# Optimization experiments

Measured on AMD Instinct MI355X. Metric: run time of the kernel, lower is better.

## Reference

```python
import jax, jax.numpy as jnp
import numpy as np

B, OBS, H, M, L1, T, A = 16384, 376, 512, 8, 3, 50, 17  # L1 = num_layers - 1
LOG_SQRT_2PI = 0.5 * np.log(2.0 * np.pi).astype(np.float32)


def setup_inputs() -> dict:
    key = jax.random.key(0)
    ks = jax.random.split(key, 16)
    s = lambda fan: 1.0 / np.sqrt(fan).astype(np.float32)
    return {
        "x": jax.random.normal(ks[0], (B, OBS), jnp.float32),
        "task_idx": jax.random.randint(ks[1], (B,), 0, T, jnp.int64),
        "enc_W1": jax.random.normal(ks[2], (OBS, H), jnp.float32) * s(OBS),
        "enc_b1": jnp.zeros((H,), jnp.float32),
        "enc_W2": jax.random.normal(ks[3], (H, H), jnp.float32) * s(H),
        "enc_b2": jnp.zeros((H,), jnp.float32),
        "task_emb": jax.random.normal(ks[4], (T, H), jnp.float32),
        "a_rW": jax.random.normal(ks[5], (L1, H, M * M), jnp.float32) * s(H),
        "a_rb": jnp.zeros((L1, M * M), jnp.float32),
        "c_rW": jax.random.normal(ks[6], (L1, H, M * M), jnp.float32) * s(H),
        "c_rb": jnp.zeros((L1, M * M), jnp.float32),
        "a_W": jax.random.normal(ks[7], (L1, M, H, H), jnp.float32) * s(H),
        "a_b": jnp.zeros((L1, M, H), jnp.float32),
        "a_Wf": jax.random.normal(ks[8], (M, H, A), jnp.float32) * 0.01,
        "a_bf": jnp.zeros((M, A), jnp.float32),
        "c_W": jax.random.normal(ks[9], (L1, M, H, H), jnp.float32) * s(H),
        "c_b": jnp.zeros((L1, M, H), jnp.float32),
        "c_Wf": jax.random.normal(ks[10], (M, H, 1), jnp.float32) * s(H),
        "c_bf": jnp.zeros((M, 1), jnp.float32),
        "actor_logstd": jnp.zeros((1, A), jnp.float32),
    }


def _routing(context, rW, rb):
    # context: [B,H]; rW: [L1,H,M*M] -> list of [B,M,M] softmax routing probs
    rel = jax.nn.relu(context)
    probs = []
    for l in range(L1):
        logits = (rel @ rW[l] + rb[l]).reshape(-1, M, M)
        probs.append(jax.nn.softmax(logits, axis=2))
    return probs


def _base(f_s, probs, W, b, Wf, bf):
    # f_s: [B,H]; W: [L1,M,H,H]; Wf: [M,H,out]
    g = jnp.broadcast_to(f_s[:, None, :], (f_s.shape[0], M, H))  # [B,M,H]
    for l in range(L1):
        outs = jax.nn.relu(jnp.einsum("bmh,mhk->bmk", g, W[l]) + b[l])  # [B,M,H]
        g = jnp.einsum("bij,bjh->bih", probs[l], outs)  # soft combine
    final = jnp.einsum("bmh,mhk->bmk", g, Wf) + bf  # [B,M,out]
    return final.sum(axis=1)


def reference(x, task_idx, enc_W1, enc_b1, enc_W2, enc_b2, task_emb,
              a_rW, a_rb, c_rW, c_rb, a_W, a_b, a_Wf, a_bf,
              c_W, c_b, c_Wf, c_bf, actor_logstd):
    f_s = jnp.tanh(jnp.tanh(x @ enc_W1 + enc_b1) @ enc_W2 + enc_b2)  # [B,H]
    h_z = task_emb[task_idx]  # [B,H]
    context = f_s * h_z

    value = _base(f_s, _routing(context, c_rW, c_rb), c_W, c_b, c_Wf, c_bf)  # [B,1]
    mean = _base(f_s, _routing(context, a_rW, a_rb), a_W, a_b, a_Wf, a_bf)   # [B,A]

    # deterministic action (sample=False): action = mean
    logstd = jnp.broadcast_to(actor_logstd, mean.shape)
    log_prob = (-logstd - LOG_SQRT_2PI).sum(axis=1)          # N.log_prob(mean).sum(1)
    entropy = (0.5 + LOG_SQRT_2PI + logstd).sum(axis=1)
    # concat (action, log_prob, entropy, value) -> [B, A+3]
    return jnp.concatenate([mean, log_prob[:, None], entropy[:, None], value], axis=1)
```

## Files before the change

### kernel.cpp

```cpp
#include <hip/hip_runtime.h>
#include <hip/hip_bf16.h>

typedef float f32x4 __attribute__((ext_vector_type(4)));
typedef float f32x2 __attribute__((ext_vector_type(2)));
typedef int   i32x4 __attribute__((ext_vector_type(4)));
typedef int   i32x8 __attribute__((ext_vector_type(8)));

#define LOG_SQRT_2PI 0.91893853320467274f

static constexpr int BSZ  = 16384;
static constexpr int OBSN = 376;
static constexpr int HD   = 512;
static constexpr int NACT = 17;

__device__ __forceinline__ unsigned char f2fp8(float v) {
  return (unsigned char)(__builtin_amdgcn_cvt_pk_fp8_f32(v, v, 0, false) & 0xFF);
}

__device__ __forceinline__ void gl16(const unsigned char* g, unsigned char* l) {
  __builtin_amdgcn_global_load_lds((const __attribute__((address_space(1))) void*)g,
                                   (__attribute__((address_space(3))) void*)l, 16, 0, 0);
}

__device__ __forceinline__ void xcd_map(int id, int gx, int gy, int& bx, int& by, int& bz) {
  int p = id & 7, l = id >> 3;
  bx = l % gx;
  int g = (l / gx) * 8 + p;
  by = g % gy;
  bz = g / gy;
}


__global__ void k_cvt_pad8(const float* __restrict__ src, unsigned char* __restrict__ dst) {
  long i = (long)blockIdx.x * 256 + threadIdx.x;
  if (i >= (long)BSZ * HD) return;
  long r = i >> 9;
  int  c = (int)(i & 511);
  dst[i] = f2fp8(c < OBSN ? src[r * OBSN + c] : 0.f);
}

__global__ void k_packT8(const float* __restrict__ src, unsigned char* __restrict__ dst,
                         int K, int N, int Kpad, long sstride, long dstride, float scale) {
  __shared__ float t[32][33];
  src += (long)blockIdx.z * sstride;
  dst += (long)blockIdx.z * dstride;
  int k0 = blockIdx.y * 32, n0 = blockIdx.x * 32;
#pragma unroll
  for (int ii = 0; ii < 4; ++ii) {
    int i = ii * 8 + threadIdx.y;
    int k = k0 + i, n = n0 + threadIdx.x;
    t[i][threadIdx.x] = (k < K && n < N) ? src[(long)k * N + n] : 0.f;
  }
  __syncthreads();
#pragma unroll
  for (int ii = 0; ii < 4; ++ii) {
    int i = ii * 8 + threadIdx.y;
    int n = n0 + i, k = k0 + threadIdx.x;
    if (n < N && k < Kpad) dst[(long)n * Kpad + k] = f2fp8(scale * t[threadIdx.x][i]);
  }
}

__global__ void k_packwF(const float* __restrict__ aW, const float* __restrict__ cW,
                         unsigned char* __restrict__ dst) {
  long i = (long)blockIdx.x * 256 + threadIdx.x;
  if (i >= (long)48 * 262144) return;
  int z = (int)(i >> 18);
  int rem = (int)(i & 262143);
  int k = rem >> 9, n = rem & 511;
  int layer = z >> 4, zz = z & 15, net = zz >> 3, m = zz & 7;
  const float* src = (net ? aW : cW) + (long)(layer * 8 + m) * 262144;
  float v = src[(long)k * 512 + n];
  int t = k >> 7, nb = n >> 4;
  int lane = ((k >> 5) & 3) * 16 + (n & 15);
  long off = ((((long)z * 4 + t) * 32 + nb) * 64 + lane) * 32 + (k & 31);
  dst[off] = f2fp8(16.f * v);
}

__global__ void k_pack_lb(const float* __restrict__ a_b, const float* __restrict__ c_b,
                          float* __restrict__ lb) {
  int i = blockIdx.x * 256 + threadIdx.x;
  if (i >= 24576) return;
  int layer = i >> 13, zz = (i >> 9) & 15, n = i & 511;
  int net = zz >> 3, m = zz & 7;
  lb[i] = (net ? a_b : c_b)[(layer * 8 + m) * 512 + n];
}

__global__ void k_packwf8(const float* __restrict__ aWf, const float* __restrict__ cWf,
                          unsigned char* __restrict__ dsta, unsigned char* __restrict__ dstc) {
  int i = blockIdx.x * 256 + threadIdx.x;
  int n = i >> 12, k = i & 4095;
  dsta[i] = (n < NACT) ? f2fp8(64.f * aWf[(long)k * NACT + n]) : (unsigned char)0;
  dstc[i] = (n < 1)    ? f2fp8(64.f * cWf[k])                  : (unsigned char)0;
}

__global__ void k_pack_rb(const float* __restrict__ a_rb, const float* __restrict__ c_rb,
                          float* __restrict__ rb) {
  int i = threadIdx.x;
  rb[i] = (i < 192) ? a_rb[i] : c_rb[i - 192];
}

__global__ void k_sum_bf(const float* __restrict__ a_bf, const float* __restrict__ c_bf,
                         float* __restrict__ sa, float* __restrict__ sc) {
  int a = threadIdx.x;
  if (a < NACT) { float s = 0.f; for (int m = 0; m < 8; ++m) s += a_bf[m * NACT + a]; sa[a] = s; }
  if (a == 0)   { float s = 0.f; for (int m = 0; m < 8; ++m) s += c_bf[m];            sc[0] = s; }
}

template <int OP>
__global__ __launch_bounds__(256, 4)
void k_gemm8(const unsigned char* __restrict__ A, const unsigned char* __restrict__ Bt,
             void* __restrict__ Cv, const float* __restrict__ bias,
             int N, int K, int lda, int ldc, int gx, int gy,
             const int* __restrict__ tidx, const float* __restrict__ temb,
             unsigned char* __restrict__ out2) {
  __shared__ alignas(16) unsigned char sA[128 * 128];
  __shared__ alignas(16) unsigned char sB[128 * 128];
  int bx, by, z;
  xcd_map(blockIdx.x, gx, gy, bx, by, z);
  const int tid  = threadIdx.x;
  const int wave = tid >> 6, lane = tid & 63;
  const int wr = (wave >> 1) * 64, wc = (wave & 1) * 64;
  const int row0 = by * 128, col0 = bx * 128;
  const int lcol = lane & 15, quad = lane >> 4;
  const int sw7 = lcol & 7;
  const int c0 = ((2 * quad)     ^ sw7) * 16;
  const int c1 = ((2 * quad + 1) ^ sw7) * 16;
  const int raA0 = (wr + lcol) * 128 + c0, raA1 = (wr + lcol) * 128 + c1;
  const int rbB0 = (wc + lcol) * 128 + c0, rbB1 = (wc + lcol) * 128 + c1;
  int aOff[4], bOff[4];
#pragma unroll
  for (int i = 0; i < 4; ++i) {
    int u = i * 256 + tid;
    int r = u >> 3, gc = (u & 7) ^ (r & 7);
    aOff[i] = (row0 + r) * lda + gc * 16;
    bOff[i] = (col0 + r) * K + gc * 16;
  }

  f32x4 acc[4][4] = {};

  for (int kt = 0; kt < K; kt += 128) {
#pragma unroll
    for (int i = 0; i < 4; ++i) gl16(A + aOff[i] + kt, &sA[i * 4096 + tid * 16]);
#pragma unroll
    for (int i = 0; i < 4; ++i) gl16(Bt + bOff[i] + kt, &sB[i * 4096 + tid * 16]);
    __syncthreads();
    i32x8 bv[4];
#pragma unroll
    for (int ni = 0; ni < 4; ++ni) {
      i32x4 blo = *(const i32x4*)&sB[rbB0 + ni * 2048];
      i32x4 bhi = *(const i32x4*)&sB[rbB1 + ni * 2048];
      bv[ni] = (i32x8){blo[0], blo[1], blo[2], blo[3], bhi[0], bhi[1], bhi[2], bhi[3]};
    }
#pragma unroll
    for (int mi = 0; mi < 4; ++mi) {
      i32x4 alo = *(const i32x4*)&sA[raA0 + mi * 2048];
      i32x4 ahi = *(const i32x4*)&sA[raA1 + mi * 2048];
      i32x8 af = (i32x8){alo[0], alo[1], alo[2], alo[3], ahi[0], ahi[1], ahi[2], ahi[3]};
#pragma unroll
      for (int ni = 0; ni < 4; ++ni)
        acc[mi][ni] = __builtin_amdgcn_mfma_scale_f32_16x16x128_f8f6f4(
            bv[ni], af, acc[mi][ni], 0, 0, 0, 0x7F, 0, 0x7F);
    }
    __syncthreads();
  }

#pragma unroll
  for (int ni = 0; ni < 4; ++ni) {
    int colb = col0 + wc + ni * 16 + quad * 4;
    if (colb >= N) continue;
    float4 bw = *(const float4*)&bias[colb];
#pragma unroll
    for (int mi = 0; mi < 4; ++mi) {
      int rowg = row0 + wr + mi * 16 + lcol;
      float v0 = acc[mi][ni][0] * 0.0625f + bw.x;
      float v1 = acc[mi][ni][1] * 0.0625f + bw.y;
      float v2 = acc[mi][ni][2] * 0.0625f + bw.z;
      float v3 = acc[mi][ni][3] * 0.0625f + bw.w;
      long idx = (long)rowg * ldc + colb;
      if (OP == 1) {
        float t0 = tanhf(v0), t1 = tanhf(v1), t2 = tanhf(v2), t3 = tanhf(v3);
        unsigned d = __builtin_amdgcn_cvt_pk_fp8_f32(t0, t1, 0, false);
        d = __builtin_amdgcn_cvt_pk_fp8_f32(t2, t3, d, true);
        *(unsigned*)&((unsigned char*)Cv)[idx] = d;
      } else if (OP == 5) {
        float t0 = tanhf(v0), t1 = tanhf(v1), t2 = tanhf(v2), t3 = tanhf(v3);
        unsigned d = __builtin_amdgcn_cvt_pk_fp8_f32(t0, t1, 0, false);
        d = __builtin_amdgcn_cvt_pk_fp8_f32(t2, t3, d, true);
        *(unsigned*)&((unsigned char*)Cv)[idx] = d;
        int tk = tidx[rowg];
        float4 te = *(const float4*)&temb[(long)tk * HD + colb];
        unsigned e = __builtin_amdgcn_cvt_pk_fp8_f32(fmaxf(t0 * te.x, 0.f), fmaxf(t1 * te.y, 0.f), 0, false);
        e = __builtin_amdgcn_cvt_pk_fp8_f32(fmaxf(t2 * te.z, 0.f), fmaxf(t3 * te.w, 0.f), e, true);
        *(unsigned*)&out2[idx] = e;
      } else if (OP == 4) {
        float mx = fmaxf(fmaxf(v0, v1), fmaxf(v2, v3));
        mx = fmaxf(mx, __shfl_xor(mx, 16));
        float e0 = __expf(v0 - mx), e1 = __expf(v1 - mx), e2 = __expf(v2 - mx), e3 = __expf(v3 - mx);
        float s = e0 + e1 + e2 + e3;
        s += __shfl_xor(s, 16);
        float inv = 1.f / s;
        *(float4*)&((float*)Cv)[idx] = make_float4(e0 * inv, e1 * inv, e2 * inv, e3 * inv);
      }
    }
  }
}

template <int AMODE>
__global__ __launch_bounds__(512, 4)
void k_gemmF(const unsigned char* __restrict__ A, const unsigned char* __restrict__ Wp,
             const float* __restrict__ lb, const float* __restrict__ probs,
             unsigned char* __restrict__ g, int gy, int poffC, int poffA) {
  __shared__ alignas(16) unsigned char sL[AMODE ? 65536 : 32768];
  int hb, slab, net;
  xcd_map(blockIdx.x, 8, gy, hb, slab, net);
  const int tid = threadIdx.x;
  const int w = tid >> 6, lane = tid & 63;
  const int lcol = lane & 15, quad = lane >> 4;
  const int ln3 = lane >> 3, sl = lane & 7;
  const int row0 = slab * 64;
  const int h0 = hb * 64;
  const int sw7 = lcol & 7;
  const int c0 = ((2 * quad)     ^ sw7) * 16;
  const int c1 = ((2 * quad + 1) ^ sw7) * 16;
  const int ch = sl ^ ln3;
  const unsigned char* wbase =
      Wp + (((long)(net * 8 + w) * 4 * 32 + hb * 4) * 64 + lane) * 32;

  f32x4 acc[4][4] = {};

  if (AMODE == 0) {
#pragma unroll
    for (int i = 0; i < 4; ++i) {
      int vb = w * 4 + i;
      int rr = (vb & 7) * 8 + ln3;
      gl16(A + (row0 + rr) * 512 + (vb >> 3) * 128 + ch * 16, &sL[(vb * 64 + lane) * 16]);
    }
    __syncthreads();
#pragma unroll
    for (int t = 0; t < 4; ++t) {
      i32x8 bv[4];
#pragma unroll
      for (int ni = 0; ni < 4; ++ni) {
        i32x4 lo = *(const i32x4*)(wbase + t * 65536 + ni * 2048);
        i32x4 hi = *(const i32x4*)(wbase + t * 65536 + ni * 2048 + 16);
        bv[ni] = (i32x8){lo[0], lo[1], lo[2], lo[3], hi[0], hi[1], hi[2], hi[3]};
      }
#pragma unroll
      for (int mi = 0; mi < 4; ++mi) {
        int ra = t * 8192 + (mi * 16 + lcol) * 128;
        i32x4 lo = *(const i32x4*)&sL[ra + c0];
        i32x4 hi = *(const i32x4*)&sL[ra + c1];
        i32x8 af = (i32x8){lo[0], lo[1], lo[2], lo[3], hi[0], hi[1], hi[2], hi[3]};
#pragma unroll
        for (int ni = 0; ni < 4; ++ni)
          acc[mi][ni] = __builtin_amdgcn_mfma_scale_f32_16x16x128_f8f6f4(
              bv[ni], af, acc[mi][ni], 0, 0, 0, 0x7F, 0, 0x7F);
      }
    }
  } else {
    const unsigned char* abase = A + (long)(row0 + ln3) * 8192 + net * 4096 + w * 512 + ch * 16;
    unsigned char* dbase = &sL[w * 8192 + lane * 16];
#pragma unroll 1
    for (int t = 0; t < 4; ++t) {
      const int kt = t * 128;
#pragma unroll
      for (int i = 0; i < 8; ++i)
        gl16(abase + i * 8 * 8192 + kt, dbase + i * 1024);
      i32x8 bv[4];
#pragma unroll
      for (int ni = 0; ni < 4; ++ni) {
        i32x4 lo = *(const i32x4*)(wbase + t * 65536 + ni * 2048);
        i32x4 hi = *(const i32x4*)(wbase + t * 65536 + ni * 2048 + 16);
        bv[ni] = (i32x8){lo[0], lo[1], lo[2], lo[3], hi[0], hi[1], hi[2], hi[3]};
      }
      asm volatile("s_waitcnt vmcnt(0)" ::: "memory");
      __builtin_amdgcn_sched_barrier(0);
#pragma unroll
      for (int mi = 0; mi < 4; ++mi) {
        int ra = w * 8192 + (mi * 16 + lcol) * 128;
        i32x4 lo = *(const i32x4*)&sL[ra + c0];
        i32x4 hi = *(const i32x4*)&sL[ra + c1];
        i32x8 af = (i32x8){lo[0], lo[1], lo[2], lo[3], hi[0], hi[1], hi[2], hi[3]};
#pragma unroll
        for (int ni = 0; ni < 4; ++ni)
          acc[mi][ni] = __builtin_amdgcn_mfma_scale_f32_16x16x128_f8f6f4(
              bv[ni], af, acc[mi][ni], 0, 0, 0, 0x7F, 0, 0x7F);
      }
    }
  }

  __syncthreads();

#pragma unroll
  for (int ni = 0; ni < 4; ++ni) {
    int col = ni * 16 + quad * 4;
    float4 bw = *(const float4*)&lb[(net * 8 + w) * 512 + h0 + col];
    int sd = ni * 4 + quad;
#pragma unroll
    for (int mi = 0; mi < 4; ++mi) {
      int row = mi * 16 + lcol;
      float v0 = fmaxf(acc[mi][ni][0] * 0.0625f + bw.x, 0.f);
      float v1 = fmaxf(acc[mi][ni][1] * 0.0625f + bw.y, 0.f);
      float v2 = fmaxf(acc[mi][ni][2] * 0.0625f + bw.z, 0.f);
      float v3 = fmaxf(acc[mi][ni][3] * 0.0625f + bw.w, 0.f);
      unsigned d = __builtin_amdgcn_cvt_pk_fp8_f32(v0, v1, 0, false);
      d = __builtin_amdgcn_cvt_pk_fp8_f32(v2, v3, d, true);
      *(unsigned*)&sL[w * 4096 + row * 64 + ((sd ^ (row & 14)) << 2)] = d;
    }
  }
  __syncthreads();

  const int poff = net ? poffA : poffC;
#pragma unroll
  for (int k = 0; k < 8; ++k) {
    const int r = k * 8 + ln3;
    const float* pr = &probs[(long)(row0 + r) * 384 + poff + w * 8];
    float4 pA = *(const float4*)pr;
    float4 pB = *(const float4*)(pr + 4);
    float p8[8] = {pA.x, pA.y, pA.z, pA.w, pB.x, pB.y, pB.z, pB.w};
    float ga[8] = {};
#pragma unroll
    for (int j = 0; j < 8; ++j) {
      uint2 o2 = *(const uint2*)&sL[j * 4096 + r * 64 + (((sl * 2) ^ (r & 14)) << 2)];
      float pw = p8[j];
      f32x2 a0 = __builtin_amdgcn_cvt_pk_f32_fp8(o2.x, false);
      f32x2 a1 = __builtin_amdgcn_cvt_pk_f32_fp8(o2.x, true);
      f32x2 a2 = __builtin_amdgcn_cvt_pk_f32_fp8(o2.y, false);
      f32x2 a3 = __builtin_amdgcn_cvt_pk_f32_fp8(o2.y, true);
      ga[0] += pw * a0.x; ga[1] += pw * a0.y; ga[2] += pw * a1.x; ga[3] += pw * a1.y;
      ga[4] += pw * a2.x; ga[5] += pw * a2.y; ga[6] += pw * a3.x; ga[7] += pw * a3.y;
    }
    unsigned lo = __builtin_amdgcn_cvt_pk_fp8_f32(ga[0], ga[1], 0, false);
    lo = __builtin_amdgcn_cvt_pk_fp8_f32(ga[2], ga[3], lo, true);
    unsigned hi = __builtin_amdgcn_cvt_pk_fp8_f32(ga[4], ga[5], 0, false);
    hi = __builtin_amdgcn_cvt_pk_fp8_f32(ga[6], ga[7], hi, true);
    *(uint2*)&g[(long)(row0 + r) * 8192 + net * 4096 + w * 512 + h0 + sl * 8] =
        make_uint2(lo, hi);
  }
}

template <int NOUT>
__global__ __launch_bounds__(256)
void k_head8(const unsigned char* __restrict__ A, const unsigned char* __restrict__ Bt,
             const float* __restrict__ bsum, float* __restrict__ out, int lda, int ooff) {
  __shared__ alignas(16) unsigned char sA[64 * 64];
  __shared__ alignas(16) unsigned char sB[32 * 64];
  const int tid = threadIdx.x;
  const int wave = tid >> 6, lane = tid & 63;
  const int row0 = blockIdx.x * 64;
  const int lcol = lane & 15, quad = lane >> 4;
  const int sw = (lcol >> 1) & 3;
  const int co0 = (((quad >> 1)    ) ^ sw) * 16 + (quad & 1) * 8;
  const int co1 = (((quad >> 1) + 2) ^ sw) * 16 + (quad & 1) * 8;
  f32x4 acc[2] = {};

  for (int kt = 0; kt < 4096; kt += 64) {
    {
      int r = tid >> 2, gc = (tid & 3) ^ ((tid >> 3) & 3);
      gl16(A + (long)(row0 + r) * lda + kt + gc * 16, &sA[tid * 16]);
    }
    if (tid < 128) {
      int r = tid >> 2, gc = (tid & 3) ^ ((tid >> 3) & 3);
      gl16(Bt + (long)r * 4096 + kt + gc * 16, &sB[tid * 16]);
    }
    __syncthreads();
    long af[2], bv[2][2];
    int ra = (wave * 16 + lcol) * 64;
    af[0] = *(const long*)&sA[ra + co0];
    af[1] = *(const long*)&sA[ra + co1];
#pragma unroll
    for (int ni = 0; ni < 2; ++ni) {
      int rbq = (ni * 16 + lcol) * 64;
      bv[0][ni] = *(const long*)&sB[rbq + co0];
      bv[1][ni] = *(const long*)&sB[rbq + co1];
    }
#pragma unroll
    for (int kk = 0; kk < 2; ++kk)
#pragma unroll
      for (int ni = 0; ni < 2; ++ni)
        acc[ni] = __builtin_amdgcn_mfma_f32_16x16x32_fp8_fp8(af[kk], bv[kk][ni], acc[ni], 0, 0, 0);
    __syncthreads();
  }

#pragma unroll
  for (int ni = 0; ni < 2; ++ni) {
    int col = ni * 16 + lcol;
    if (col >= NOUT) continue;
#pragma unroll
    for (int r = 0; r < 4; ++r) {
      int row = row0 + wave * 16 + quad * 4 + r;
      out[(long)row * 20 + ooff + col] = acc[ni][r] * 0.015625f + bsum[col];
    }
  }
}

__global__ void k_logstd(const float* __restrict__ ls, float* __restrict__ out) {
  float lp = 0.f, ent = 0.f;
#pragma unroll
  for (int a = 0; a < NACT; ++a) {
    float v = ls[a];
    lp  += -v - LOG_SQRT_2PI;
    ent += 0.5f + LOG_SQRT_2PI + v;
  }
  long b = (long)blockIdx.x * 256 + threadIdx.x;
  if (b < BSZ) { out[b * 20 + 17] = lp; out[b * 20 + 18] = ent; }
}


extern "C" void kernel_launch(void* const* d_in, const int* in_sizes, int n_in,
                              void* d_out, int out_size, void* d_ws, size_t ws_size,
                              hipStream_t stream) {
  const float* x        = (const float*)d_in[0];
  const int*   task_idx = (const int*)d_in[1];
  const float* enc_W1   = (const float*)d_in[2];
  const float* enc_b1   = (const float*)d_in[3];
  const float* enc_W2   = (const float*)d_in[4];
  const float* enc_b2   = (const float*)d_in[5];
  const float* task_emb = (const float*)d_in[6];
  const float* a_rW     = (const float*)d_in[7];
  const float* a_rb     = (const float*)d_in[8];
  const float* c_rW     = (const float*)d_in[9];
  const float* c_rb     = (const float*)d_in[10];
  const float* a_W      = (const float*)d_in[11];
  const float* a_b      = (const float*)d_in[12];
  const float* a_Wf     = (const float*)d_in[13];
  const float* a_bf     = (const float*)d_in[14];
  const float* c_W      = (const float*)d_in[15];
  const float* c_b      = (const float*)d_in[16];
  const float* c_Wf     = (const float*)d_in[17];
  const float* c_bf     = (const float*)d_in[18];
  const float* logstd   = (const float*)d_in[19];
  float* out = (float*)d_out;

  char* ws = (char*)d_ws;
  size_t off = 0;
  auto carve = [&](size_t bytes) {
    char* p = ws + off;
    off += (bytes + 255) & ~(size_t)255;
    return p;
  };
  unsigned char* W8 = (unsigned char*)carve((size_t)48 * 262144);
  unsigned char* W1T8 = (unsigned char*)carve((size_t)512 * 512);
  unsigned char* W2T8 = (unsigned char*)carve((size_t)512 * 512);
  unsigned char* rWT8 = (unsigned char*)carve((size_t)384 * 512);
  float* rball = (float*)carve(384 * 4);
  float* lb    = (float*)carve(3 * 16 * 512 * 4);
  unsigned char* WfaT8 = (unsigned char*)carve((size_t)32 * 4096);
  unsigned char* WfcT8 = (unsigned char*)carve((size_t)32 * 4096);
  float* bfa   = (float*)carve(128 * 4);
  float* bfc   = (float*)carve(128 * 4);
  unsigned char* fs8 = (unsigned char*)carve((size_t)BSZ * HD);
  float* lgt   = (float*)carve((size_t)BSZ * 384 * 4);

  size_t remain = (ws_size > off) ? (ws_size - off) : 0;
  int Bc = 2048;
  for (int cand = BSZ; cand > 2048; cand >>= 1)
    if ((size_t)2 * cand * 8192 <= remain) { Bc = cand; break; }
  size_t half = (size_t)Bc * 8192;
  unsigned char* bufA8 = (unsigned char*)carve(half);
  unsigned char* bufB8 = (unsigned char*)carve(half);
  unsigned char* x8   = bufA8;
  unsigned char* h18  = bufB8;
  unsigned char* rel8 = bufA8;

  dim3 tb(32, 8);

  k_cvt_pad8<<<(int)(((long)BSZ * HD + 255) / 256), 256, 0, stream>>>(x, x8);
  k_packT8<<<dim3(16, 16, 1), tb, 0, stream>>>(enc_W1, W1T8, OBSN, 512, 512, 0, 0, 16.f);
  k_packT8<<<dim3(16, 16, 1), tb, 0, stream>>>(enc_W2, W2T8, 512, 512, 512, 0, 0, 16.f);
  k_packT8<<<dim3(2, 16, 3),  tb, 0, stream>>>(a_rW, rWT8,             512, 64, 512, 512 * 64, 64 * 512, 16.f);
  k_packT8<<<dim3(2, 16, 3),  tb, 0, stream>>>(c_rW, rWT8 + 192 * 512, 512, 64, 512, 512 * 64, 64 * 512, 16.f);
  k_packwF<<<(int)(((long)48 * 262144 + 255) / 256), 256, 0, stream>>>(a_W, c_W, W8);
  k_pack_lb<<<96, 256, 0, stream>>>(a_b, c_b, lb);
  k_packwf8<<<512, 256, 0, stream>>>(a_Wf, c_Wf, WfaT8, WfcT8);
  k_pack_rb<<<1, 384, 0, stream>>>(a_rb, c_rb, rball);
  k_sum_bf<<<1, 32, 0, stream>>>(a_bf, c_bf, bfa, bfc);

  const int GY = BSZ / 128;
  k_gemm8<1><<<4 * GY, 256, 0, stream>>>(x8, W1T8, h18, enc_b1, 512, 512, 512, 512,
                                         4, GY, nullptr, nullptr, nullptr);
  k_gemm8<5><<<4 * GY, 256, 0, stream>>>(h18, W2T8, fs8, enc_b2, 512, 512, 512, 512,
                                         4, GY, task_idx, task_emb, rel8);
  k_gemm8<4><<<3 * GY, 256, 0, stream>>>(rel8, rWT8, lgt, rball, 384, 512, 512, 384,
                                         3, GY, nullptr, nullptr, nullptr);

  const size_t wlz = (size_t)16 * 262144;
  for (int c0 = 0; c0 < BSZ; c0 += Bc) {
    const unsigned char* fs_c = fs8 + (long)c0 * 512;
    const float* pr_c  = lgt + (long)c0 * 384;
    float*       out_c = out + (long)c0 * 20;
    const int gyF = Bc / 64;

    k_gemmF<0><<<16 * gyF, 512, 0, stream>>>(fs_c, W8, lb, pr_c, bufA8, gyF, 192, 0);
    k_gemmF<1><<<16 * gyF, 512, 0, stream>>>(bufA8, W8 + wlz, lb + 8192, pr_c, bufB8,
                                             gyF, 192 + 64, 64);
    k_gemmF<1><<<16 * gyF, 512, 0, stream>>>(bufB8, W8 + 2 * wlz, lb + 16384, pr_c, bufA8,
                                             gyF, 192 + 128, 128);
    k_head8<1><<<Bc / 64, 256, 0, stream>>>(bufA8, WfcT8, bfc, out_c, 8192, 19);
    k_head8<NACT><<<Bc / 64, 256, 0, stream>>>(bufA8 + 4096, WfaT8, bfa, out_c, 8192, 0);
  }

  k_logstd<<<BSZ / 256, 256, 0, stream>>>(logstd, out);
}
```

Measured before the change: 757.5 us.

## Fuse final head projections into last mixture layer with atomic accumulation

The last k_gemmF layer now keeps its combined fp8 activations in shared memory and applies the actor and critic final projections there. Partial sums from each hidden-column block are added into the output with atomicAdd, and a new init kernel writes the summed biases into the output first. This removes the two k_head8 launches and the write and re-read of the final layer activations. The intermediate g layout and the Wf packing are permuted so that each block holds a contiguous k-slice. The cost is extra atomics, a non-deterministic float summation order, and more shared memory use in the fused kernel.

After: 739.5 us. 1.02x faster.

```diff
diff --git a/kernel.cpp b/kernel.cpp
--- a/kernel.cpp
+++ b/kernel.cpp
@@ -88,9 +88,11 @@
 __global__ void k_packwf8(const float* __restrict__ aWf, const float* __restrict__ cWf,
                           unsigned char* __restrict__ dsta, unsigned char* __restrict__ dstc) {
   int i = blockIdx.x * 256 + threadIdx.x;
-  int n = i >> 12, k = i & 4095;
-  dsta[i] = (n < NACT) ? f2fp8(64.f * aWf[(long)k * NACT + n]) : (unsigned char)0;
-  dstc[i] = (n < 1)    ? f2fp8(64.f * cWf[k])                  : (unsigned char)0;
+  int n = i >> 12, kn = i & 4095;
+  int hb = kn >> 9, rem = kn & 511, m = rem >> 6, u = kn & 63;
+  int ko = m * 512 + hb * 64 + u;
+  dsta[i] = (n < NACT) ? f2fp8(64.f * aWf[(long)ko * NACT + n]) : (unsigned char)0;
+  dstc[i] = (n < 1)    ? f2fp8(64.f * cWf[ko])                  : (unsigned char)0;
 }
 
 __global__ void k_pack_rb(const float* __restrict__ a_rb, const float* __restrict__ c_rb,
@@ -104,6 +106,14 @@
   int a = threadIdx.x;
   if (a < NACT) { float s = 0.f; for (int m = 0; m < 8; ++m) s += a_bf[m * NACT + a]; sa[a] = s; }
   if (a == 0)   { float s = 0.f; for (int m = 0; m < 8; ++m) s += c_bf[m];            sc[0] = s; }
+}
+
+__global__ void k_initout(const float* __restrict__ bfa, const float* __restrict__ bfc,
+                          float* __restrict__ out) {
+  long i = (long)blockIdx.x * 256 + threadIdx.x;
+  if (i >= (long)BSZ * 20) return;
+  int o = (int)(i % 20);
+  out[i] = (o < NACT) ? bfa[o] : (o == 19 ? bfc[0] : 0.f);
 }
 
 template <int OP>
@@ -205,11 +215,13 @@
   }
 }
 
-template <int AMODE>
+template <int AMODE, int HEAD>
 __global__ __launch_bounds__(512, 4)
 void k_gemmF(const unsigned char* __restrict__ A, const unsigned char* __restrict__ Wp,
              const float* __restrict__ lb, const float* __restrict__ probs,
-             unsigned char* __restrict__ g, int gy, int poffC, int poffA) {
+             unsigned char* __restrict__ g, int gy, int poffC, int poffA,
+             const unsigned char* __restrict__ Wfc, const unsigned char* __restrict__ Wfa,
+             float* __restrict__ outp) {
   __shared__ alignas(16) unsigned char sL[AMODE ? 65536 : 32768];
   int hb, slab, net;
   xcd_map(blockIdx.x, 8, gy, hb, slab, net);
@@ -258,14 +270,14 @@
       }
     }
   } else {
-    const unsigned char* abase = A + (long)(row0 + ln3) * 8192 + net * 4096 + w * 512 + ch * 16;
+    const unsigned char* abase = A + (long)(row0 + ln3) * 8192 + net * 4096 +
+                                 w * 64 + (ch >> 2) * 512 + (ch & 3) * 16;
     unsigned char* dbase = &sL[w * 8192 + lane * 16];
 #pragma unroll 1
     for (int t = 0; t < 4; ++t) {
-      const int kt = t * 128;
 #pragma unroll
       for (int i = 0; i < 8; ++i)
-        gl16(abase + i * 8 * 8192 + kt, dbase + i * 1024);
+        gl16(abase + i * 8 * 8192 + t * 1024, dbase + i * 1024);
       i32x8 bv[4];
 #pragma unroll
       for (int ni = 0; ni < 4; ++ni) {
@@ -334,62 +346,47 @@
     lo = __builtin_amdgcn_cvt_pk_fp8_f32(ga[2], ga[3], lo, true);
     unsigned hi = __builtin_amdgcn_cvt_pk_fp8_f32(ga[4], ga[5], 0, false);
     hi = __builtin_amdgcn_cvt_pk_fp8_f32(ga[6], ga[7], hi, true);
-    *(uint2*)&g[(long)(row0 + r) * 8192 + net * 4096 + w * 512 + h0 + sl * 8] =
-        make_uint2(lo, hi);
-  }
-}
-
-template <int NOUT>
-__global__ __launch_bounds__(256)
-void k_head8(const unsigned char* __restrict__ A, const unsigned char* __restrict__ Bt,
-             const float* __restrict__ bsum, float* __restrict__ out, int lda, int ooff) {
-  __shared__ alignas(16) unsigned char sA[64 * 64];
-  __shared__ alignas(16) unsigned char sB[32 * 64];
-  const int tid = threadIdx.x;
-  const int wave = tid >> 6, lane = tid & 63;
-  const int row0 = blockIdx.x * 64;
-  const int lcol = lane & 15, quad = lane >> 4;
-  const int sw = (lcol >> 1) & 3;
-  const int co0 = (((quad >> 1)    ) ^ sw) * 16 + (quad & 1) * 8;
-  const int co1 = (((quad >> 1) + 2) ^ sw) * 16 + (quad & 1) * 8;
-  f32x4 acc[2] = {};
-
-  for (int kt = 0; kt < 4096; kt += 64) {
-    {
-      int r = tid >> 2, gc = (tid & 3) ^ ((tid >> 3) & 3);
-      gl16(A + (long)(row0 + r) * lda + kt + gc * 16, &sA[tid * 16]);
-    }
-    if (tid < 128) {
-      int r = tid >> 2, gc = (tid & 3) ^ ((tid >> 3) & 3);
-      gl16(Bt + (long)r * 4096 + kt + gc * 16, &sB[tid * 16]);
-    }
+    if (HEAD) {
+      *(uint2*)&sL[32768 + w * 4096 + r * 64 + (((sl * 2) ^ (r & 14)) << 2)] =
+          make_uint2(lo, hi);
+    } else {
+      *(uint2*)&g[(long)(row0 + r) * 8192 + net * 4096 + hb * 512 + w * 64 + sl * 8] =
+          make_uint2(lo, hi);
+    }
+  }
+
+  if (HEAD) {
     __syncthreads();
-    long af[2], bv[2][2];
-    int ra = (wave * 16 + lcol) * 64;
-    af[0] = *(const long*)&sA[ra + co0];
-    af[1] = *(const long*)&sA[ra + co1];
+    const unsigned char* Wf = net ? Wfa : Wfc;
+    const int ooff = net ? 0 : 19;
+    const int mi = w & 3, kh = w >> 2;
+    const int hrow = mi * 16 + lcol;
+    f32x4 hacc[2] = {};
+#pragma unroll
+    for (int ks = 0; ks < 8; ++ks) {
+      int j = kh * 4 + (ks >> 1);
+      int u = (ks & 1) * 32 + quad * 8;
+      int sd = u >> 2;
+      long af = *(const long*)&sL[32768 + j * 4096 + hrow * 64 + ((sd ^ (hrow & 14)) << 2)];
+      int kglob = hb * 512 + kh * 256 + ks * 32 + quad * 8;
+      long bv0 = *(const long*)&Wf[(long)lcol * 4096 + kglob];
+      hacc[0] = __builtin_amdgcn_mfma_f32_16x16x32_fp8_fp8(af, bv0, hacc[0], 0, 0, 0);
+      if (net) {
+        long bv1 = *(const long*)&Wf[(long)(16 + lcol) * 4096 + kglob];
+        hacc[1] = __builtin_amdgcn_mfma_f32_16x16x32_fp8_fp8(af, bv1, hacc[1], 0, 0, 0);
+      }
+    }
+    const int NOUTn = net ? NACT : 1;
 #pragma unroll
     for (int ni = 0; ni < 2; ++ni) {
-      int rbq = (ni * 16 + lcol) * 64;
-      bv[0][ni] = *(const long*)&sB[rbq + co0];
-      bv[1][ni] = *(const long*)&sB[rbq + co1];
-    }
-#pragma unroll
-    for (int kk = 0; kk < 2; ++kk)
-#pragma unroll
-      for (int ni = 0; ni < 2; ++ni)
-        acc[ni] = __builtin_amdgcn_mfma_f32_16x16x32_fp8_fp8(af[kk], bv[kk][ni], acc[ni], 0, 0, 0);
-    __syncthreads();
-  }
-
-#pragma unroll
-  for (int ni = 0; ni < 2; ++ni) {
-    int col = ni * 16 + lcol;
-    if (col >= NOUT) continue;
-#pragma unroll
-    for (int r = 0; r < 4; ++r) {
-      int row = row0 + wave * 16 + quad * 4 + r;
-      out[(long)row * 20 + ooff + col] = acc[ni][r] * 0.015625f + bsum[col];
+      if (ni == 1 && !net) break;
+      int col = ni * 16 + lcol;
+      if (col >= NOUTn) continue;
+#pragma unroll
+      for (int rr = 0; rr < 4; ++rr) {
+        int row = row0 + mi * 16 + quad * 4 + rr;
+        atomicAdd(&outp[(long)row * 20 + ooff + col], hacc[ni][rr] * 0.015625f);
+      }
     }
   }
 }
@@ -475,6 +472,7 @@
   k_packwf8<<<512, 256, 0, stream>>>(a_Wf, c_Wf, WfaT8, WfcT8);
   k_pack_rb<<<1, 384, 0, stream>>>(a_rb, c_rb, rball);
   k_sum_bf<<<1, 32, 0, stream>>>(a_bf, c_bf, bfa, bfc);
+  k_initout<<<(int)(((long)BSZ * 20 + 255) / 256), 256, 0, stream>>>(bfa, bfc, out);
 
   const int GY = BSZ / 128;
   k_gemm8<1><<<4 * GY, 256, 0, stream>>>(x8, W1T8, h18, enc_b1, 512, 512, 512, 512,
@@ -491,13 +489,12 @@
     float*       out_c = out + (long)c0 * 20;
     const int gyF = Bc / 64;
 
-    k_gemmF<0><<<16 * gyF, 512, 0, stream>>>(fs_c, W8, lb, pr_c, bufA8, gyF, 192, 0);
-    k_gemmF<1><<<16 * gyF, 512, 0, stream>>>(bufA8, W8 + wlz, lb + 8192, pr_c, bufB8,
-                                             gyF, 192 + 64, 64);
-    k_gemmF<1><<<16 * gyF, 512, 0, stream>>>(bufB8, W8 + 2 * wlz, lb + 16384, pr_c, bufA8,
-                                             gyF, 192 + 128, 128);
-    k_head8<1><<<Bc / 64, 256, 0, stream>>>(bufA8, WfcT8, bfc, out_c, 8192, 19);
-    k_head8<NACT><<<Bc / 64, 256, 0, stream>>>(bufA8 + 4096, WfaT8, bfa, out_c, 8192, 0);
+    k_gemmF<0, 0><<<16 * gyF, 512, 0, stream>>>(fs_c, W8, lb, pr_c, bufA8, gyF, 192, 0,
+                                                nullptr, nullptr, nullptr);
+    k_gemmF<1, 0><<<16 * gyF, 512, 0, stream>>>(bufA8, W8 + wlz, lb + 8192, pr_c, bufB8,
+                                                gyF, 192 + 64, 64, nullptr, nullptr, nullptr);
+    k_gemmF<1, 1><<<16 * gyF, 512, 0, stream>>>(bufB8, W8 + 2 * wlz, lb + 16384, pr_c, bufA8,
+                                                gyF, 192 + 128, 128, WfcT8, WfaT8, out_c);
   }
 
   k_logstd<<<BSZ / 256, 256, 0, stream>>>(logstd, out);
```
